# Optimization experiments

Hardware: AMD Instinct MI355X
Metric: run time of the kernel (lower is better)

The kernel has to match this reference:

```python
import jax, jax.numpy as jnp
import numpy as np

D_MODEL = 1024
NUM_HEADS = 16
D_K = D_MODEL // NUM_HEADS


def setup_inputs() -> dict:
    key = jax.random.key(0)
    ks = jax.random.split(key, 9)
    s = 1.0 / np.sqrt(D_MODEL)
    x = jax.random.normal(ks[0], (4, 2048, D_MODEL), dtype=jnp.float32)
    Wq = jax.random.uniform(ks[1], (D_MODEL, D_MODEL), jnp.float32, -s, s)
    bq = jax.random.uniform(ks[2], (D_MODEL,), jnp.float32, -s, s)
    Wk = jax.random.uniform(ks[3], (D_MODEL, D_MODEL), jnp.float32, -s, s)
    bk = jax.random.uniform(ks[4], (D_MODEL,), jnp.float32, -s, s)
    Wv = jax.random.uniform(ks[5], (D_MODEL, D_MODEL), jnp.float32, -s, s)
    bv = jax.random.uniform(ks[6], (D_MODEL,), jnp.float32, -s, s)
    Wo = jax.random.uniform(ks[7], (D_MODEL, D_MODEL), jnp.float32, -s, s)
    bo = jax.random.uniform(ks[8], (D_MODEL,), jnp.float32, -s, s)
    return {"x": x, "Wq": Wq, "bq": bq, "Wk": Wk, "bk": bk,
            "Wv": Wv, "bv": bv, "Wo": Wo, "bo": bo}


def reference(x, Wq, bq, Wk, bk, Wv, bv, Wo, bo):
    B, T, C = x.shape
    H, Dk = NUM_HEADS, D_K
    # linear projections (torch Linear: x @ W.T + b; here W stored as [in,out])
    q = (x @ Wq + bq).reshape(B, T, H, Dk).transpose(0, 2, 1, 3)  # [B,H,T,Dk]
    k = (x @ Wk + bk).reshape(B, T, H, Dk).transpose(0, 2, 1, 3)
    v = (x @ Wv + bv).reshape(B, T, H, Dk).transpose(0, 2, 1, 3)
    scores = jnp.einsum("bhtd,bhsd->bhts", q, k) / jnp.sqrt(jnp.float32(Dk))
    attn = jax.nn.softmax(scores, axis=-1)  # [B,H,T,T]
    context = jnp.einsum("bhts,bhsd->bhtd", attn, v)
    context = context.transpose(0, 2, 1, 3).reshape(B, T, C)
    return context @ Wo + bo
```

## Files before the change

### kernel.cpp

```cpp
#include <hip/hip_runtime.h>
#include <hip/hip_bf16.h>
#include <stdint.h>

typedef short bf16x8 __attribute__((ext_vector_type(8)));
typedef float f32x4  __attribute__((ext_vector_type(4)));

#define MFMA16(a, b, c) __builtin_amdgcn_mfma_f32_16x16x32_bf16((a), (b), (c), 0, 0, 0)

__device__ __forceinline__ unsigned short f2bf(float f) {
    union { float f; unsigned int u; } v; v.f = f;
    unsigned int u = v.u;
    u += 0x7fffu + ((u >> 16) & 1u);
    return (unsigned short)(u >> 16);
}

__device__ __forceinline__ unsigned int trunc_pk(float a, float b) {
    return (__float_as_uint(a) >> 16) | (__float_as_uint(b) & 0xffff0000u);
}

__device__ __forceinline__ float exp2f_fast(float x) {
#if __has_builtin(__builtin_amdgcn_exp2f)
    return __builtin_amdgcn_exp2f(x);
#else
    return exp2f(x);
#endif
}

__device__ __forceinline__ void g2lds16(const void* g, void* l) {
    __builtin_amdgcn_global_load_lds(
        (const __attribute__((address_space(1))) void*)g,
        (__attribute__((address_space(3))) void*)l, 16, 0, 0);
}


__global__ __launch_bounds__(256) void convert_x_kernel(
    const float4* __restrict__ src, ushort4* __restrict__ dst)
{
    int i = blockIdx.x * 256 + threadIdx.x;
    float4 v = src[i];
    ushort4 o;
    o.x = f2bf(v.x); o.y = f2bf(v.y); o.z = f2bf(v.z); o.w = f2bf(v.w);
    dst[i] = o;
}

__global__ __launch_bounds__(256) void transpose_w_kernel(
    const float* __restrict__ src, unsigned short* __restrict__ dst)
{
    __shared__ float tile[64][65];
    const int k0 = blockIdx.x * 64, n0 = blockIdx.y * 64;
    const int tx = threadIdx.x & 63, ty = threadIdx.x >> 6;
    #pragma unroll
    for (int i = 0; i < 64; i += 4)
        tile[ty + i][tx] = src[(size_t)(k0 + ty + i) * 1024 + n0 + tx];
    __syncthreads();
    #pragma unroll
    for (int i = 0; i < 64; i += 4)
        dst[(size_t)(n0 + ty + i) * 1024 + k0 + tx] = f2bf(tile[tx][ty + i]);
}


#define QSCALE 0.18033688011112042f

template <int MODE>
__global__ __launch_bounds__(256, 2) void gemm_bt(
    const unsigned short* __restrict__ A, const unsigned short* __restrict__ Bt,
    const float* __restrict__ b0, const float* __restrict__ b1, const float* __restrict__ b2,
    unsigned short* __restrict__ Qb, unsigned short* __restrict__ Kb,
    unsigned short* __restrict__ Vt, float* __restrict__ out)
{
    __shared__ alignas(16) unsigned short As[128 * 32];
    __shared__ alignas(16) unsigned short Bs[128 * 32];

    const int t = threadIdx.x;
    const int m0 = blockIdx.y * 128, n0 = blockIdx.x * 128;
    const int lane = t & 63, w = t >> 6, quad = lane >> 4, c16 = lane & 15;
    const int moff = (w >> 1) * 64, noff = (w & 1) * 64;

    f32x4 acc[4][4];
    #pragma unroll
    for (int i = 0; i < 4; ++i)
        #pragma unroll
        for (int j = 0; j < 4; ++j)
            acc[i][j] = (f32x4){0.f, 0.f, 0.f, 0.f};

    const unsigned short* Ag = A + (size_t)(m0 + (t >> 2)) * 1024 + (t & 3) * 8;
    const unsigned short* Bg = Bt + (size_t)(n0 + (t >> 2)) * 1024 + (t & 3) * 8;
    unsigned short* Asl = As + t * 8;
    unsigned short* Bsl = Bs + t * 8;

    for (int k0 = 0; k0 < 1024; k0 += 32) {
        g2lds16(Ag + k0,             Asl);
        g2lds16(Ag + 64 * 1024 + k0, Asl + 2048);
        g2lds16(Bg + k0,             Bsl);
        g2lds16(Bg + 64 * 1024 + k0, Bsl + 2048);
        __syncthreads();

        bf16x8 af[4], bfr[4];
        #pragma unroll
        for (int ms = 0; ms < 4; ++ms)
            af[ms] = *(const bf16x8*)(As + (moff + ms * 16 + c16) * 32 + quad * 8);
        #pragma unroll
        for (int ns = 0; ns < 4; ++ns)
            bfr[ns] = *(const bf16x8*)(Bs + (noff + ns * 16 + c16) * 32 + quad * 8);
        #pragma unroll
        for (int ms = 0; ms < 4; ++ms)
            #pragma unroll
            for (int ns = 0; ns < 4; ++ns)
                acc[ms][ns] = MFMA16(af[ms], bfr[ns], acc[ms][ns]);
        __syncthreads();
    }

    #pragma unroll
    for (int ns = 0; ns < 4; ++ns) {
        const int n = n0 + noff + ns * 16 + c16;
        if (MODE == 0) {
            const int mat = n >> 10, nn = n & 1023;
            const int h = nn >> 6, d = nn & 63;
            const float bias = (mat == 0) ? b0[nn] : ((mat == 1) ? b1[nn] : b2[nn]);
            #pragma unroll
            for (int ms = 0; ms < 4; ++ms) {
                const int mbase = m0 + moff + ms * 16 + quad * 4;
                const int b = mbase >> 11, tbase = mbase & 2047;
                const int bh = b * 16 + h;
                if (mat == 2) {
                    ushort4 pk;
                    pk.x = f2bf(acc[ms][ns][0] + bias);
                    pk.y = f2bf(acc[ms][ns][1] + bias);
                    pk.z = f2bf(acc[ms][ns][2] + bias);
                    pk.w = f2bf(acc[ms][ns][3] + bias);
                    *(ushort4*)(Vt + ((size_t)bh * 64 + d) * 2048 + tbase) = pk;
                } else {
                    #pragma unroll
                    for (int r = 0; r < 4; ++r) {
                        float v = acc[ms][ns][r] + bias;
                        if (mat == 0) v *= QSCALE;
                        unsigned short* dst = (mat == 0) ? Qb : Kb;
                        dst[((size_t)bh * 2048 + tbase + r) * 64 + d] = f2bf(v);
                    }
                }
            }
        } else {
            const float bias = b0[n];
            #pragma unroll
            for (int ms = 0; ms < 4; ++ms) {
                #pragma unroll
                for (int r = 0; r < 4; ++r) {
                    const int m = m0 + moff + ms * 16 + quad * 4 + r;
                    out[(size_t)m * 1024 + n] = acc[ms][ns][r] + bias;
                }
            }
        }
    }
}


__global__ __launch_bounds__(128, 2) void attn_kernel(
    const unsigned short* __restrict__ Qb, const unsigned short* __restrict__ Kb,
    const unsigned short* __restrict__ Vt, unsigned short* __restrict__ ctx)
{
    __shared__ alignas(16) unsigned short Ks[64 * 64];
    __shared__ alignas(16) unsigned short Vs[64 * 64];

    const int t = threadIdx.x, w = t >> 6, lane = t & 63;
    const int quad = lane >> 4, c16 = lane & 15;
    const int bh = blockIdx.y;
    const int qbase = blockIdx.x * 128 + w * 64;

    bf16x8 qf[4][2];
    #pragma unroll
    for (int mt = 0; mt < 4; ++mt) {
        const unsigned short* Qp = Qb + ((size_t)bh * 2048 + qbase + mt * 16 + c16) * 64;
        qf[mt][0] = *(const bf16x8*)(Qp + quad * 8);
        qf[mt][1] = *(const bf16x8*)(Qp + 32 + quad * 8);
    }

    float l_r[4] = {0.f, 0.f, 0.f, 0.f};
    f32x4 O[4][4];
    #pragma unroll
    for (int mt = 0; mt < 4; ++mt)
        #pragma unroll
        for (int dc = 0; dc < 4; ++dc) O[mt][dc] = (f32x4){0.f, 0.f, 0.f, 0.f};

    const int sgrp = (t & 7) ^ ((t >> 3) & 7);
    const unsigned short* Kgl = Kb + (size_t)bh * 131072 + (size_t)(t >> 3) * 64 + sgrp * 8;
    const unsigned short* Vgl = Vt + (size_t)bh * 131072 + (size_t)(t >> 3) * 2048 + sgrp * 8;
    unsigned short* Ksl = Ks + t * 8;
    unsigned short* Vsl = Vs + t * 8;
    const f32x4 fzero = {0.f, 0.f, 0.f, 0.f};

    for (int s0 = 0; s0 < 2048; s0 += 64) {
        #pragma unroll
        for (int q = 0; q < 4; ++q) {
            g2lds16(Kgl + s0 * 64 + q * 1024,  Ksl + q * 1024);
            g2lds16(Vgl + s0 + q * 32768,      Vsl + q * 1024);
        }
        __syncthreads();

        #pragma unroll
        for (int ct = 0; ct < 4; ++ct) {
            const int key = ct * 16 + c16;
            const bf16x8 kf0 = *(const bf16x8*)(Ks + key * 64 + ((quad ^ (key & 7)) << 3));
            const bf16x8 kf1 = *(const bf16x8*)(Ks + key * 64 + (((4 + quad) ^ (key & 7)) << 3));

            uint2 vf[4];
            const int g = ct * 2 + (quad >> 1);
            #pragma unroll
            for (int dc = 0; dc < 4; ++dc) {
                const int d = dc * 16 + c16;
                vf[dc] = *(const uint2*)(Vs + d * 64 + ((g ^ (d & 7)) << 3) + (quad & 1) * 4);
            }

            #pragma unroll
            for (int mt = 0; mt < 4; ++mt) {
                f32x4 sa = MFMA16(kf0, qf[mt][0], fzero);
                sa = MFMA16(kf1, qf[mt][1], sa);
                const float p0 = exp2f_fast(sa[0]);
                const float p1 = exp2f_fast(sa[1]);
                const float p2 = exp2f_fast(sa[2]);
                const float p3 = exp2f_fast(sa[3]);
                l_r[mt] += (p0 + p1) + (p2 + p3);
                union { bf16x8 v; unsigned int d[4]; } af;
                af.d[0] = trunc_pk(p0, p1);
                af.d[1] = trunc_pk(p2, p3);
                af.d[2] = 0u; af.d[3] = 0u;
                #pragma unroll
                for (int dc = 0; dc < 4; ++dc) {
                    union { bf16x8 v; uint2 u[2]; } bfv;
                    bfv.u[0] = vf[dc]; bfv.u[1] = vf[dc];
                    O[mt][dc] = MFMA16(af.v, bfv.v, O[mt][dc]);
                }
            }
        }
        __syncthreads();
    }

    #pragma unroll
    for (int mt = 0; mt < 4; ++mt) {
        l_r[mt] += __shfl_xor(l_r[mt], 16);
        l_r[mt] += __shfl_xor(l_r[mt], 32);
    }

    const int b = bh >> 4, h = bh & 15;
    #pragma unroll
    for (int mt = 0; mt < 4; ++mt) {
        float inv[4];
        #pragma unroll
        for (int r = 0; r < 4; ++r)
            inv[r] = 1.0f / __shfl(l_r[mt], quad * 4 + r);
        #pragma unroll
        for (int dc = 0; dc < 4; ++dc)
            #pragma unroll
            for (int r = 0; r < 4; ++r) {
                const int row = qbase + mt * 16 + quad * 4 + r;
                ctx[((size_t)(b * 2048 + row)) * 1024 + h * 64 + dc * 16 + c16] =
                    f2bf(O[mt][dc][r] * inv[r]);
            }
    }
}


extern "C" void kernel_launch(void* const* d_in, const int* in_sizes, int n_in,
                              void* d_out, int out_size, void* d_ws, size_t ws_size,
                              hipStream_t stream)
{
    const float* x  = (const float*)d_in[0];
    const float* Wq = (const float*)d_in[1];
    const float* bq = (const float*)d_in[2];
    const float* Wk = (const float*)d_in[3];
    const float* bk = (const float*)d_in[4];
    const float* Wv = (const float*)d_in[5];
    const float* bv = (const float*)d_in[6];
    const float* Wo = (const float*)d_in[7];
    const float* bo = (const float*)d_in[8];
    float* out = (float*)d_out;

    char* ws = (char*)d_ws;
    unsigned short* xb    = (unsigned short*)(ws);
    unsigned short* Wqkvt = (unsigned short*)(ws + (16u << 20));
    unsigned short* Wot   = (unsigned short*)(ws + (22u << 20));
    unsigned short* Vt    = (unsigned short*)(ws + (24u << 20));
    unsigned short* Qb    = (unsigned short*)((char*)d_out);
    unsigned short* Kb    = (unsigned short*)((char*)d_out + (16u << 20));

    convert_x_kernel<<<8192, 256, 0, stream>>>((const float4*)x, (ushort4*)xb);
    dim3 tg(16, 16);
    transpose_w_kernel<<<tg, 256, 0, stream>>>(Wq, Wqkvt);
    transpose_w_kernel<<<tg, 256, 0, stream>>>(Wk, Wqkvt + (1u << 20));
    transpose_w_kernel<<<tg, 256, 0, stream>>>(Wv, Wqkvt + (2u << 20));
    transpose_w_kernel<<<tg, 256, 0, stream>>>(Wo, Wot);

    gemm_bt<0><<<dim3(24, 64), 256, 0, stream>>>(xb, Wqkvt, bq, bk, bv, Qb, Kb, Vt, nullptr);
    attn_kernel<<<dim3(16, 64), 128, 0, stream>>>(Qb, Kb, Vt, xb );
    gemm_bt<1><<<dim3(8, 64), 256, 0, stream>>>(xb, Wot, bo, nullptr, nullptr,
                                                nullptr, nullptr, nullptr, out);
}
```

Before: 303.0 us.

## Double-buffer attention K/V loads with single-wave blocks and merge weight transposes

The attention kernel now runs one wave per block and double-buffers the K/V tiles in LDS. The next tile's global-to-LDS loads are issued before the current tile is computed, and the block barriers are replaced with vmcnt waits, aiming to hide load latency. Blocks are remapped so that neighbouring blocks share the same batch-head K/V data, which should improve L2 reuse. The four weight-transpose launches are merged into one launch over a z-dimension to cut launch overhead. The wait relies on the wave's own vmcnt ordering, and each block now uses twice the LDS.

```diff
diff --git a/kernel.cpp b/kernel.cpp
--- a/kernel.cpp
+++ b/kernel.cpp
@@ -43,10 +43,15 @@
     dst[i] = o;
 }
 
-__global__ __launch_bounds__(256) void transpose_w_kernel(
-    const float* __restrict__ src, unsigned short* __restrict__ dst)
+__global__ __launch_bounds__(256) void transpose_w4_kernel(
+    const float* __restrict__ W0, const float* __restrict__ W1,
+    const float* __restrict__ W2, const float* __restrict__ W3,
+    unsigned short* __restrict__ dst_base)
 {
     __shared__ float tile[64][65];
+    const int z = blockIdx.z;
+    const float* src = (z == 0) ? W0 : (z == 1) ? W1 : (z == 2) ? W2 : W3;
+    unsigned short* dst = dst_base + ((size_t)z << 20);
     const int k0 = blockIdx.x * 64, n0 = blockIdx.y * 64;
     const int tx = threadIdx.x & 63, ty = threadIdx.x >> 6;
     #pragma unroll
@@ -154,17 +159,19 @@
 }
 
 
-__global__ __launch_bounds__(128, 2) void attn_kernel(
+__global__ __launch_bounds__(64) void attn_kernel(
     const unsigned short* __restrict__ Qb, const unsigned short* __restrict__ Kb,
     const unsigned short* __restrict__ Vt, unsigned short* __restrict__ ctx)
 {
-    __shared__ alignas(16) unsigned short Ks[64 * 64];
-    __shared__ alignas(16) unsigned short Vs[64 * 64];
-
-    const int t = threadIdx.x, w = t >> 6, lane = t & 63;
-    const int quad = lane >> 4, c16 = lane & 15;
-    const int bh = blockIdx.y;
-    const int qbase = blockIdx.x * 128 + w * 64;
+    __shared__ alignas(16) unsigned short Ks[2][64 * 64];
+    __shared__ alignas(16) unsigned short Vs[2][64 * 64];
+
+    const int t = threadIdx.x;
+    const int quad = t >> 4, c16 = t & 15;
+    const int L = blockIdx.y * 32 + blockIdx.x;
+    const int bh = ((L & 7) << 3) + (L >> 8);
+    const int qt = (L >> 3) & 31;
+    const int qbase = qt * 64;
 
     bf16x8 qf[4][2];
     #pragma unroll
@@ -181,33 +188,48 @@
         #pragma unroll
         for (int dc = 0; dc < 4; ++dc) O[mt][dc] = (f32x4){0.f, 0.f, 0.f, 0.f};
 
-    const int sgrp = (t & 7) ^ ((t >> 3) & 7);
-    const unsigned short* Kgl = Kb + (size_t)bh * 131072 + (size_t)(t >> 3) * 64 + sgrp * 8;
-    const unsigned short* Vgl = Vt + (size_t)bh * 131072 + (size_t)(t >> 3) * 2048 + sgrp * 8;
-    unsigned short* Ksl = Ks + t * 8;
-    unsigned short* Vsl = Vs + t * 8;
+    const int srow = t >> 3;
+    const int sg = (t & 7) ^ (srow & 7);
+    const unsigned short* Kg = Kb + (size_t)bh * 131072 + (size_t)srow * 64 + sg * 8;
+    const unsigned short* Vg = Vt + (size_t)bh * 131072 + (size_t)srow * 2048 + sg * 8;
     const f32x4 fzero = {0.f, 0.f, 0.f, 0.f};
 
-    for (int s0 = 0; s0 < 2048; s0 += 64) {
-        #pragma unroll
-        for (int q = 0; q < 4; ++q) {
-            g2lds16(Kgl + s0 * 64 + q * 1024,  Ksl + q * 1024);
-            g2lds16(Vgl + s0 + q * 32768,      Vsl + q * 1024);
+    #pragma unroll
+    for (int j = 0; j < 8; ++j) {
+        g2lds16(Kg + j * 512, &Ks[0][t * 8 + j * 512]);
+        g2lds16(Vg + (size_t)j * 16384, &Vs[0][t * 8 + j * 512]);
+    }
+
+    for (int s = 0; s < 32; ++s) {
+        const int buf = s & 1;
+        if (s < 31) {
+            const unsigned short* kc = Kg + (size_t)(s + 1) * 4096;
+            const unsigned short* vc = Vg + (size_t)(s + 1) * 64;
+            #pragma unroll
+            for (int j = 0; j < 8; ++j) {
+                g2lds16(kc + j * 512, &Ks[buf ^ 1][t * 8 + j * 512]);
+                g2lds16(vc + (size_t)j * 16384, &Vs[buf ^ 1][t * 8 + j * 512]);
+            }
+            asm volatile("s_waitcnt vmcnt(16)" ::: "memory");
+        } else {
+            asm volatile("s_waitcnt vmcnt(0)" ::: "memory");
         }
-        __syncthreads();
+
+        const unsigned short* Ksb = Ks[buf];
+        const unsigned short* Vsb = Vs[buf];
 
         #pragma unroll
         for (int ct = 0; ct < 4; ++ct) {
             const int key = ct * 16 + c16;
-            const bf16x8 kf0 = *(const bf16x8*)(Ks + key * 64 + ((quad ^ (key & 7)) << 3));
-            const bf16x8 kf1 = *(const bf16x8*)(Ks + key * 64 + (((4 + quad) ^ (key & 7)) << 3));
+            const bf16x8 kf0 = *(const bf16x8*)(Ksb + key * 64 + ((quad ^ (key & 7)) << 3));
+            const bf16x8 kf1 = *(const bf16x8*)(Ksb + key * 64 + (((4 + quad) ^ (key & 7)) << 3));
 
             uint2 vf[4];
             const int g = ct * 2 + (quad >> 1);
             #pragma unroll
             for (int dc = 0; dc < 4; ++dc) {
                 const int d = dc * 16 + c16;
-                vf[dc] = *(const uint2*)(Vs + d * 64 + ((g ^ (d & 7)) << 3) + (quad & 1) * 4);
+                vf[dc] = *(const uint2*)(Vsb + d * 64 + ((g ^ (d & 7)) << 3) + (quad & 1) * 4);
             }
 
             #pragma unroll
@@ -231,7 +253,6 @@
                 }
             }
         }
-        __syncthreads();
     }
 
     #pragma unroll
@@ -277,20 +298,16 @@
     char* ws = (char*)d_ws;
     unsigned short* xb    = (unsigned short*)(ws);
     unsigned short* Wqkvt = (unsigned short*)(ws + (16u << 20));
-    unsigned short* Wot   = (unsigned short*)(ws + (22u << 20));
     unsigned short* Vt    = (unsigned short*)(ws + (24u << 20));
+    unsigned short* Wot   = Wqkvt + (3u << 20);
     unsigned short* Qb    = (unsigned short*)((char*)d_out);
     unsigned short* Kb    = (unsigned short*)((char*)d_out + (16u << 20));
 
     convert_x_kernel<<<8192, 256, 0, stream>>>((const float4*)x, (ushort4*)xb);
-    dim3 tg(16, 16);
-    transpose_w_kernel<<<tg, 256, 0, stream>>>(Wq, Wqkvt);
-    transpose_w_kernel<<<tg, 256, 0, stream>>>(Wk, Wqkvt + (1u << 20));
-    transpose_w_kernel<<<tg, 256, 0, stream>>>(Wv, Wqkvt + (2u << 20));
-    transpose_w_kernel<<<tg, 256, 0, stream>>>(Wo, Wot);
+    transpose_w4_kernel<<<dim3(16, 16, 4), 256, 0, stream>>>(Wq, Wk, Wv, Wo, Wqkvt);
 
     gemm_bt<0><<<dim3(24, 64), 256, 0, stream>>>(xb, Wqkvt, bq, bk, bv, Qb, Kb, Vt, nullptr);
-    attn_kernel<<<dim3(16, 64), 128, 0, stream>>>(Qb, Kb, Vt, xb );
+    attn_kernel<<<dim3(32, 64), 64, 0, stream>>>(Qb, Kb, Vt, xb );
     gemm_bt<1><<<dim3(8, 64), 256, 0, stream>>>(xb, Wot, bo, nullptr, nullptr,
                                                 nullptr, nullptr, nullptr, out);
 }
```

Measured after the change: 388.1 us. 28.1% more time.
